# Optimization experiments

Hardware: AMD Instinct MI355X
Metric: run time of the kernel (lower is better)

The kernel has to match this reference:

```python
import jax, jax.numpy as jnp
import numpy as np

EPS = 1e-7  # K.epsilon()

def squash(s):
    # s: [B, J, D]
    sq_norm = jnp.sum(jnp.square(s), axis=-1, keepdims=True)
    scale = sq_norm / (1.0 + sq_norm) / jnp.sqrt(sq_norm + EPS)
    return scale * s

def setup_inputs() -> dict:
    key = jax.random.key(0)
    k1, k2 = jax.random.split(key)
    B, I, Din = 128, 2048, 8
    J, D = 16, 16
    inputs = jax.random.normal(k1, (B, I, Din), dtype=jnp.float32)
    # glorot-uniform-ish scale for W
    limit = np.sqrt(6.0 / (Din + D)).astype(np.float32)
    W = jax.random.uniform(k2, (J, I, D, Din), dtype=jnp.float32, minval=-limit, maxval=limit)
    return {"inputs": inputs, "W": W}

def reference(inputs, W):
    # inputs: [B, I, Din]; W: [J, I, D, Din]
    num_routings = 3
    # inputs_hat[b,j,i,d] = sum_f W[j,i,d,f] * inputs[b,i,f]
    u_hat = jnp.einsum('bif,jidf->bjid', inputs, W)  # [B, J, I, D]
    B, J, I, D = u_hat.shape
    b = jnp.zeros((B, J, I), dtype=u_hat.dtype)
    v = None
    for r in range(num_routings):
        c = jax.nn.softmax(b, axis=1)                 # softmax over output capsules (dim=1)
        s = jnp.einsum('bji,bjid->bjd', c, u_hat)     # weighted sum over input capsules
        v = squash(s)                                 # [B, J, D]
        if r < num_routings - 1:
            b = b + jnp.einsum('bjd,bjid->bji', v, u_hat)  # agreement update
    return v
```

## Files before the change

### kernel.cpp

```cpp
#include <hip/hip_runtime.h>
#include <math.h>

#define B_   128
#define I_   2048
#define F_   8
#define J_   16
#define D_   16
#define JD   256
#define IT   16
#define NIT  (I_/IT)
#define BT   16
#define NBT  (B_/BT)
#define SROW 257

typedef _Float16 f16;
typedef _Float16 f16x8 __attribute__((ext_vector_type(8)));
typedef _Float16 f16x4 __attribute__((ext_vector_type(4)));
typedef float    f32x4 __attribute__((ext_vector_type(4)));

#if defined(__has_builtin)
#  if __has_builtin(__builtin_amdgcn_permlane32_swap)
#    define HAVE_PLS32 1
#  endif
#endif

template <int CTRL>
__device__ __forceinline__ float dpp_add(float v) {
    int t = __builtin_amdgcn_update_dpp(0, __float_as_int(v), CTRL, 0xF, 0xF, true);
    return v + __int_as_float(t);
}
__device__ __forceinline__ float row_sum16(float v) {
    v = dpp_add<0x128>(v);
    v = dpp_add<0x124>(v);
    v = dpp_add<0x122>(v);
    v = dpp_add<0x121>(v);
    return v;
}

__device__ __forceinline__ float fold16(float p) {
    return p + __int_as_float(__builtin_amdgcn_ds_swizzle(__float_as_int(p), 0x401F));
}
__device__ __forceinline__ float fold32(float p) {
#ifdef HAVE_PLS32
    auto r = __builtin_amdgcn_permlane32_swap(__float_as_int(p), __float_as_int(p),
                                              false, false);
    return __int_as_float(r[0]) + __int_as_float(r[1]);
#else
    return p + __shfl_xor(p, 32);
#endif
}

__global__ __launch_bounds__(256) void cvt_f16(const float* __restrict__ W,
                                               const float* __restrict__ x,
                                               f16* __restrict__ Wt,
                                               f16* __restrict__ xt) {
    const size_t NW = (size_t)J_ * I_ * D_ * F_;
    const size_t NX = (size_t)B_ * I_ * F_;
    size_t k = ((size_t)blockIdx.x * 256 + threadIdx.x) * 4;
    if (k < NW) {
        float4 a = *reinterpret_cast<const float4*>(W + k);
        f16x4 h = {(f16)a.x, (f16)a.y, (f16)a.z, (f16)a.w};
        *reinterpret_cast<f16x4*>(Wt + k) = h;
    } else {
        size_t k2 = k - NW;
        if (k2 < NX) {
            float4 a = *reinterpret_cast<const float4*>(x + k2);
            f16x4 h = {(f16)a.x, (f16)a.y, (f16)a.z, (f16)a.w};
            *reinterpret_cast<f16x4*>(xt + k2) = h;
        }
    }
}

template <int PASS>
__global__ __launch_bounds__(256) void caps_pass(
    const f16* __restrict__ Wt,
    const f16* __restrict__ xt,
    const float* __restrict__ vsum,
    f16* __restrict__ sp)
{
    const int it = blockIdx.x, bg = blockIdx.y;
    const int i0 = it * IT, b0 = bg * BT;
    const int t = threadIdx.x;
    const int w = t >> 6, l = t & 63;
    const int lb = l & 15, lq = l >> 4;

    __shared__ f16   xlds[IT][BT][F_];
    __shared__ float cl[PASS ? (J_ * IT * BT) : 1];
    __shared__ float slds[BT * SROW];

    {
        const int b = t >> 4, i = t & 15;
        f16x8 v = *reinterpret_cast<const f16x8*>(
            xt + ((size_t)(b0 + b) * I_ + i0 + i) * F_);
        *reinterpret_cast<f16x8*>(&xlds[i][b][0]) = v;
    }

    const f16* wp[4];
    #pragma unroll
    for (int jj = 0; jj < 4; ++jj)
        wp[jj] = Wt + (((size_t)(w * 4 + jj) * I_ + i0) * D_ + lb) * F_;

    f32x4 zero = {0.f, 0.f, 0.f, 0.f};
    f32x4 sacc[4] = {zero, zero, zero, zero};

    if constexpr (PASS == 1) {
        float4 vr[4];
        #pragma unroll
        for (int jj = 0; jj < 4; ++jj)
            vr[jj] = *reinterpret_cast<const float4*>(
                vsum + (size_t)(b0 + lb) * JD + (w * 4 + jj) * D_ + lq * 4);
        __syncthreads();

        #pragma unroll 4
        for (int il = 0; il < IT; ++il) {
            f16x8 bf = {0, 0, 0, 0, 0, 0, 0, 0};
            if (l < 16) bf = *reinterpret_cast<const f16x8*>(&xlds[il][lb][0]);
            #pragma unroll
            for (int jj = 0; jj < 4; ++jj) {
                f16x8 af = *reinterpret_cast<const f16x8*>(wp[jj] + il * (D_ * F_));
                f32x4 u = __builtin_amdgcn_mfma_f32_16x16x32_f16(af, bf, zero, 0, 0, 0);
                float p = u[0] * vr[jj].x + u[1] * vr[jj].y +
                          u[2] * vr[jj].z + u[3] * vr[jj].w;
                p = fold32(fold16(p));
                if (l < 16) cl[(((w * 4 + jj) * IT) + il) * BT + lb] = p;
            }
        }
        __syncthreads();

        {
            const int i = t >> 4, b = t & 15;
            float e[J_];
            float mx = -1e30f;
            #pragma unroll
            for (int j = 0; j < J_; ++j) {
                e[j] = cl[(j * IT + i) * BT + b];
                mx = fmaxf(mx, e[j]);
            }
            float s = 0.f;
            #pragma unroll
            for (int j = 0; j < J_; ++j) { e[j] = __expf(e[j] - mx); s += e[j]; }
            const float inv = 1.f / s;
            #pragma unroll
            for (int j = 0; j < J_; ++j) cl[(j * IT + i) * BT + b] = e[j] * inv;
        }
        __syncthreads();
    } else {
        __syncthreads();
    }

    #pragma unroll
    for (int m = 0; m < 4; ++m) {
        const int i = m * 4 + lq;
        f16x8 xf = *reinterpret_cast<const f16x8*>(&xlds[i][lb][0]);
        #pragma unroll
        for (int jj = 0; jj < 4; ++jj) {
            f16x8 bf;
            if constexpr (PASS == 1) {
                const float cf = cl[(((w * 4 + jj) * IT) + i) * BT + lb];
                const f16 ch = (f16)cf;
                bf = xf * ch;
            } else {
                bf = xf;
            }
            f16x8 af = *reinterpret_cast<const f16x8*>(wp[jj] + i * (D_ * F_));
            sacc[jj] = __builtin_amdgcn_mfma_f32_16x16x32_f16(af, bf, sacc[jj], 0, 0, 0);
        }
    }

    #pragma unroll
    for (int jj = 0; jj < 4; ++jj) {
        if constexpr (PASS == 0) sacc[jj] *= 0.0625f;
        const int j = w * 4 + jj;
        #pragma unroll
        for (int r = 0; r < 4; ++r)
            slds[lb * SROW + j * D_ + lq * 4 + r] = sacc[jj][r];
    }
    __syncthreads();
    {
        const int b = t >> 4, seg = t & 15;
        float o[16];
        #pragma unroll
        for (int k = 0; k < 16; ++k)
            o[k] = slds[b * SROW + seg * 16 + k];
        f16x8 o0 = {(f16)o[0], (f16)o[1], (f16)o[2],  (f16)o[3],
                    (f16)o[4], (f16)o[5], (f16)o[6],  (f16)o[7]};
        f16x8 o1 = {(f16)o[8], (f16)o[9], (f16)o[10], (f16)o[11],
                    (f16)o[12], (f16)o[13], (f16)o[14], (f16)o[15]};
        f16* dst = sp + ((size_t)it * B_ + b0 + b) * JD + seg * 16;
        *reinterpret_cast<f16x8*>(dst) = o0;
        *reinterpret_cast<f16x8*>(dst + 8) = o1;
    }
}

template <int MODE>
__global__ __launch_bounds__(512) void caps_reduce(
    const f16* __restrict__ sp,
    const float* __restrict__ vA,
    float* __restrict__ vout)
{
    const int b = blockIdx.x;
    const int t = threadIdx.x;
    const int jd = t & 255, h = t >> 8;

    float acc = 0.f;
    const f16* p = sp + ((size_t)(h * 64) * B_ + b) * JD + jd;
    #pragma unroll 16
    for (int i = 0; i < 64; ++i)
        acc += (float)p[(size_t)i * B_ * JD];

    __shared__ float red[256];
    if (h) red[jd] = acc;
    __syncthreads();
    if (!h) {
        acc += red[jd];
        const float sq = row_sum16(acc * acc);
        const float scale = sq / (1.f + sq) * rsqrtf(sq + 1e-7f);
        float v = scale * acc;
        if (MODE == 1) v += vA[(size_t)b * JD + jd];
        vout[(size_t)b * JD + jd] = v;
    }
}

extern "C" void kernel_launch(void* const* d_in, const int* in_sizes, int n_in,
                              void* d_out, int out_size, void* d_ws,
                              size_t ws_size, hipStream_t stream) {
    const float* x = (const float*)d_in[0];
    const float* W = (const float*)d_in[1];
    float* out = (float*)d_out;

    f16* Wt = (f16*)d_ws;
    f16* xt = Wt + (size_t)J_ * I_ * D_ * F_;
    f16* sp = xt + (size_t)B_ * I_ * F_;
    float* vA = (float*)(sp + (size_t)NIT * B_ * JD);
    float* vB = vA + (size_t)B_ * JD;

    const int TOT4 = (int)(((size_t)J_ * I_ * D_ * F_ + (size_t)B_ * I_ * F_) / 4);
    cvt_f16<<<TOT4 / 256, 256, 0, stream>>>(W, x, Wt, xt);

    dim3 grid(NIT, NBT), blk(256);

    caps_pass<0><<<grid, blk, 0, stream>>>(Wt, xt, nullptr, sp);
    caps_reduce<0><<<B_, 512, 0, stream>>>(sp, nullptr, vA);
    caps_pass<1><<<grid, blk, 0, stream>>>(Wt, xt, vA, sp);
    caps_reduce<1><<<B_, 512, 0, stream>>>(sp, vA, vB);
    caps_pass<1><<<grid, blk, 0, stream>>>(Wt, xt, vB, sp);
    caps_reduce<2><<<B_, 512, 0, stream>>>(sp, nullptr, out);
}
```

Measured before the change: 80.28 us.

## Replace partial-sum buffers and reduce kernels with fp32 atomics and fused squash

Each routing pass now accumulates its per-tile s contributions straight into fp32 global buffers with hardware float atomics, instead of writing fp16 partials that a separate reduce kernel then summed. The squash (and the running sum of v across iterations) is recomputed at the start of each pass from the raw s buffers, so only one small final squash kernel remains and a memset clears the accumulators. This cuts two kernel launches and the partial-buffer round trip, but adds atomic contention: 128 tiles add into each element. It also adds redundant squash work in every block and makes the accumulation order nondeterministic.

Result: slower. 214.1 us (+166.8%).

```diff
diff --git a/kernel.cpp b/kernel.cpp
--- a/kernel.cpp
+++ b/kernel.cpp
@@ -11,7 +11,7 @@
 #define NIT  (I_/IT)
 #define BT   16
 #define NBT  (B_/BT)
-#define SROW 257
+#define VROW 260
 
 typedef _Float16 f16;
 typedef _Float16 f16x8 __attribute__((ext_vector_type(8)));
@@ -47,6 +47,14 @@
     return __int_as_float(r[0]) + __int_as_float(r[1]);
 #else
     return p + __shfl_xor(p, 32);
+#endif
+}
+
+__device__ __forceinline__ void atomic_add_f32(float* p, float v) {
+#if defined(__AMDGCN__)
+    asm volatile("global_atomic_add_f32 %0, %1, off" :: "v"(p), "v"(v) : "memory");
+#else
+    atomicAdd(p, v);
 #endif
 }
 
@@ -75,8 +83,9 @@
 __global__ __launch_bounds__(256) void caps_pass(
     const f16* __restrict__ Wt,
     const f16* __restrict__ xt,
-    const float* __restrict__ vsum,
-    f16* __restrict__ sp)
+    const float* __restrict__ vS0,
+    const float* __restrict__ vS1,
+    float* __restrict__ vSo)
 {
     const int it = blockIdx.x, bg = blockIdx.y;
     const int i0 = it * IT, b0 = bg * BT;
@@ -86,7 +95,7 @@
 
     __shared__ f16   xlds[IT][BT][F_];
     __shared__ float cl[PASS ? (J_ * IT * BT) : 1];
-    __shared__ float slds[BT * SROW];
+    __shared__ float vlds[PASS ? (BT * VROW) : 1];
 
     {
         const int b = t >> 4, i = t & 15;
@@ -95,6 +104,45 @@
         *reinterpret_cast<f16x8*>(&xlds[i][b][0]) = v;
     }
 
+    if constexpr (PASS >= 1) {
+        const int b = t >> 4, j = t & 15;
+        const float* p0 = vS0 + (size_t)(b0 + b) * JD + j * D_;
+        float s[16], v[16];
+        #pragma unroll
+        for (int q = 0; q < 4; ++q) {
+            float4 a = *reinterpret_cast<const float4*>(p0 + q * 4);
+            s[q * 4 + 0] = a.x; s[q * 4 + 1] = a.y;
+            s[q * 4 + 2] = a.z; s[q * 4 + 3] = a.w;
+        }
+        float sq = 0.f;
+        #pragma unroll
+        for (int d = 0; d < 16; ++d) sq = fmaf(s[d], s[d], sq);
+        float scale = sq / (1.f + sq) * rsqrtf(sq + 1e-7f);
+        #pragma unroll
+        for (int d = 0; d < 16; ++d) v[d] = scale * s[d];
+        if constexpr (PASS == 2) {
+            const float* p1 = vS1 + (size_t)(b0 + b) * JD + j * D_;
+            #pragma unroll
+            for (int q = 0; q < 4; ++q) {
+                float4 a = *reinterpret_cast<const float4*>(p1 + q * 4);
+                s[q * 4 + 0] = a.x; s[q * 4 + 1] = a.y;
+                s[q * 4 + 2] = a.z; s[q * 4 + 3] = a.w;
+            }
+            sq = 0.f;
+            #pragma unroll
+            for (int d = 0; d < 16; ++d) sq = fmaf(s[d], s[d], sq);
+            scale = sq / (1.f + sq) * rsqrtf(sq + 1e-7f);
+            #pragma unroll
+            for (int d = 0; d < 16; ++d) v[d] += scale * s[d];
+        }
+        #pragma unroll
+        for (int q = 0; q < 4; ++q) {
+            float4 a = {v[q * 4 + 0], v[q * 4 + 1], v[q * 4 + 2], v[q * 4 + 3]};
+            *reinterpret_cast<float4*>(&vlds[b * VROW + j * D_ + q * 4]) = a;
+        }
+    }
+    __syncthreads();
+
     const f16* wp[4];
     #pragma unroll
     for (int jj = 0; jj < 4; ++jj)
@@ -103,13 +151,12 @@
     f32x4 zero = {0.f, 0.f, 0.f, 0.f};
     f32x4 sacc[4] = {zero, zero, zero, zero};
 
-    if constexpr (PASS == 1) {
+    if constexpr (PASS >= 1) {
         float4 vr[4];
         #pragma unroll
         for (int jj = 0; jj < 4; ++jj)
             vr[jj] = *reinterpret_cast<const float4*>(
-                vsum + (size_t)(b0 + lb) * JD + (w * 4 + jj) * D_ + lq * 4);
-        __syncthreads();
+                &vlds[lb * VROW + (w * 4 + jj) * D_ + lq * 4]);
 
         #pragma unroll 4
         for (int il = 0; il < IT; ++il) {
@@ -136,15 +183,13 @@
                 e[j] = cl[(j * IT + i) * BT + b];
                 mx = fmaxf(mx, e[j]);
             }
-            float s = 0.f;
-            #pragma unroll
-            for (int j = 0; j < J_; ++j) { e[j] = __expf(e[j] - mx); s += e[j]; }
-            const float inv = 1.f / s;
+            float ssum = 0.f;
+            #pragma unroll
+            for (int j = 0; j < J_; ++j) { e[j] = __expf(e[j] - mx); ssum += e[j]; }
+            const float inv = 1.f / ssum;
             #pragma unroll
             for (int j = 0; j < J_; ++j) cl[(j * IT + i) * BT + b] = e[j] * inv;
         }
-        __syncthreads();
-    } else {
         __syncthreads();
     }
 
@@ -155,7 +200,7 @@
         #pragma unroll
         for (int jj = 0; jj < 4; ++jj) {
             f16x8 bf;
-            if constexpr (PASS == 1) {
+            if constexpr (PASS >= 1) {
                 const float cf = cl[(((w * 4 + jj) * IT) + i) * BT + lb];
                 const f16 ch = (f16)cf;
                 bf = xf * ch;
@@ -170,55 +215,21 @@
     #pragma unroll
     for (int jj = 0; jj < 4; ++jj) {
         if constexpr (PASS == 0) sacc[jj] *= 0.0625f;
-        const int j = w * 4 + jj;
+        float* base = vSo + (size_t)(b0 + lb) * JD + (w * 4 + jj) * D_ + lq * 4;
         #pragma unroll
         for (int r = 0; r < 4; ++r)
-            slds[lb * SROW + j * D_ + lq * 4 + r] = sacc[jj][r];
-    }
-    __syncthreads();
-    {
-        const int b = t >> 4, seg = t & 15;
-        float o[16];
-        #pragma unroll
-        for (int k = 0; k < 16; ++k)
-            o[k] = slds[b * SROW + seg * 16 + k];
-        f16x8 o0 = {(f16)o[0], (f16)o[1], (f16)o[2],  (f16)o[3],
-                    (f16)o[4], (f16)o[5], (f16)o[6],  (f16)o[7]};
-        f16x8 o1 = {(f16)o[8], (f16)o[9], (f16)o[10], (f16)o[11],
-                    (f16)o[12], (f16)o[13], (f16)o[14], (f16)o[15]};
-        f16* dst = sp + ((size_t)it * B_ + b0 + b) * JD + seg * 16;
-        *reinterpret_cast<f16x8*>(dst) = o0;
-        *reinterpret_cast<f16x8*>(dst + 8) = o1;
-    }
-}
-
-template <int MODE>
-__global__ __launch_bounds__(512) void caps_reduce(
-    const f16* __restrict__ sp,
-    const float* __restrict__ vA,
-    float* __restrict__ vout)
-{
+            atomic_add_f32(base + r, sacc[jj][r]);
+    }
+}
+
+__global__ __launch_bounds__(256) void sq_out(const float* __restrict__ vS2,
+                                              float* __restrict__ out) {
     const int b = blockIdx.x;
     const int t = threadIdx.x;
-    const int jd = t & 255, h = t >> 8;
-
-    float acc = 0.f;
-    const f16* p = sp + ((size_t)(h * 64) * B_ + b) * JD + jd;
-    #pragma unroll 16
-    for (int i = 0; i < 64; ++i)
-        acc += (float)p[(size_t)i * B_ * JD];
-
-    __shared__ float red[256];
-    if (h) red[jd] = acc;
-    __syncthreads();
-    if (!h) {
-        acc += red[jd];
-        const float sq = row_sum16(acc * acc);
-        const float scale = sq / (1.f + sq) * rsqrtf(sq + 1e-7f);
-        float v = scale * acc;
-        if (MODE == 1) v += vA[(size_t)b * JD + jd];
-        vout[(size_t)b * JD + jd] = v;
-    }
+    const float s = vS2[(size_t)b * JD + t];
+    const float sq = row_sum16(s * s);
+    const float scale = sq / (1.f + sq) * rsqrtf(sq + 1e-7f);
+    out[(size_t)b * JD + t] = scale * s;
 }
 
 extern "C" void kernel_launch(void* const* d_in, const int* in_sizes, int n_in,
@@ -230,19 +241,19 @@
 
     f16* Wt = (f16*)d_ws;
     f16* xt = Wt + (size_t)J_ * I_ * D_ * F_;
-    f16* sp = xt + (size_t)B_ * I_ * F_;
-    float* vA = (float*)(sp + (size_t)NIT * B_ * JD);
-    float* vB = vA + (size_t)B_ * JD;
+    float* vS0 = (float*)(xt + (size_t)B_ * I_ * F_);
+    float* vS1 = vS0 + (size_t)B_ * JD;
+    float* vS2 = vS1 + (size_t)B_ * JD;
+
+    hipMemsetAsync(vS0, 0, 3 * (size_t)B_ * JD * sizeof(float), stream);
 
     const int TOT4 = (int)(((size_t)J_ * I_ * D_ * F_ + (size_t)B_ * I_ * F_) / 4);
     cvt_f16<<<TOT4 / 256, 256, 0, stream>>>(W, x, Wt, xt);
 
     dim3 grid(NIT, NBT), blk(256);
 
-    caps_pass<0><<<grid, blk, 0, stream>>>(Wt, xt, nullptr, sp);
-    caps_reduce<0><<<B_, 512, 0, stream>>>(sp, nullptr, vA);
-    caps_pass<1><<<grid, blk, 0, stream>>>(Wt, xt, vA, sp);
-    caps_reduce<1><<<B_, 512, 0, stream>>>(sp, vA, vB);
-    caps_pass<1><<<grid, blk, 0, stream>>>(Wt, xt, vB, sp);
-    caps_reduce<2><<<B_, 512, 0, stream>>>(sp, nullptr, out);
-}
+    caps_pass<0><<<grid, blk, 0, stream>>>(Wt, xt, nullptr, nullptr, vS0);
+    caps_pass<1><<<grid, blk, 0, stream>>>(Wt, xt, vS0, nullptr, vS1);
+    caps_pass<2><<<grid, blk, 0, stream>>>(Wt, xt, vS0, vS1, vS2);
+    sq_out<<<B_, 256, 0, stream>>>(vS2, out);
+}
```

## Halve input-capsule tile, share LDS via union, vectorize split partial reduction

Applied to the files above, without the earlier changes.

The input-capsule tile size becomes a template parameter. When the workspace is large enough, the passes run with 8 capsules per block instead of 16, which doubles the number of blocks. The routing-logit buffer and the output staging buffer now share one LDS union, guarded by an extra barrier, to cut shared-memory use per block. The reduce kernel is split across two blocks per batch row, loads eight f16 values per vector load and reduces 32 groups through LDS. The costs are twice the partial-sum traffic through global memory and a larger workspace requirement; if the workspace is too small, the old 16-capsule tile is used.

Result: no change. 81.59 us (+1.6%).

```diff
diff --git a/kernel.cpp b/kernel.cpp
--- a/kernel.cpp
+++ b/kernel.cpp
@@ -7,8 +7,6 @@
 #define J_   16
 #define D_   16
 #define JD   256
-#define IT   16
-#define NIT  (I_/IT)
 #define BT   16
 #define NBT  (B_/BT)
 #define SROW 257
@@ -71,7 +69,7 @@
     }
 }
 
-template <int PASS>
+template <int IT, int PASS>
 __global__ __launch_bounds__(256) void caps_pass(
     const f16* __restrict__ Wt,
     const f16* __restrict__ xt,
@@ -84,15 +82,24 @@
     const int w = t >> 6, l = t & 63;
     const int lb = l & 15, lq = l >> 4;
 
-    __shared__ f16   xlds[IT][BT][F_];
-    __shared__ float cl[PASS ? (J_ * IT * BT) : 1];
-    __shared__ float slds[BT * SROW];
-
-    {
+    __shared__ f16 xlds[IT][BT][F_];
+    __shared__ union {
+        float cl[J_ * IT * BT];
+        float slds[BT * SROW];
+    } sh;
+
+    if constexpr (IT == 16) {
         const int b = t >> 4, i = t & 15;
         f16x8 v = *reinterpret_cast<const f16x8*>(
             xt + ((size_t)(b0 + b) * I_ + i0 + i) * F_);
         *reinterpret_cast<f16x8*>(&xlds[i][b][0]) = v;
+    } else {
+        if (t < 128) {
+            const int b = t >> 3, i = t & 7;
+            f16x8 v = *reinterpret_cast<const f16x8*>(
+                xt + ((size_t)(b0 + b) * I_ + i0 + i) * F_);
+            *reinterpret_cast<f16x8*>(&xlds[i][b][0]) = v;
+        }
     }
 
     const f16* wp[4];
@@ -122,41 +129,41 @@
                 float p = u[0] * vr[jj].x + u[1] * vr[jj].y +
                           u[2] * vr[jj].z + u[3] * vr[jj].w;
                 p = fold32(fold16(p));
-                if (l < 16) cl[(((w * 4 + jj) * IT) + il) * BT + lb] = p;
+                if (l < 16) sh.cl[(((w * 4 + jj) * IT) + il) * BT + lb] = p;
             }
         }
         __syncthreads();
 
-        {
+        if (t < IT * BT) {
             const int i = t >> 4, b = t & 15;
             float e[J_];
             float mx = -1e30f;
             #pragma unroll
             for (int j = 0; j < J_; ++j) {
-                e[j] = cl[(j * IT + i) * BT + b];
+                e[j] = sh.cl[(j * IT + i) * BT + b];
                 mx = fmaxf(mx, e[j]);
             }
-            float s = 0.f;
-            #pragma unroll
-            for (int j = 0; j < J_; ++j) { e[j] = __expf(e[j] - mx); s += e[j]; }
-            const float inv = 1.f / s;
-            #pragma unroll
-            for (int j = 0; j < J_; ++j) cl[(j * IT + i) * BT + b] = e[j] * inv;
-        }
-        __syncthreads();
-    } else {
-        __syncthreads();
-    }
-
-    #pragma unroll
-    for (int m = 0; m < 4; ++m) {
+            float ssum = 0.f;
+            #pragma unroll
+            for (int j = 0; j < J_; ++j) { e[j] = __expf(e[j] - mx); ssum += e[j]; }
+            const float inv = 1.f / ssum;
+            #pragma unroll
+            for (int j = 0; j < J_; ++j) sh.cl[(j * IT + i) * BT + b] = e[j] * inv;
+        }
+        __syncthreads();
+    } else {
+        __syncthreads();
+    }
+
+    #pragma unroll
+    for (int m = 0; m < IT / 4; ++m) {
         const int i = m * 4 + lq;
         f16x8 xf = *reinterpret_cast<const f16x8*>(&xlds[i][lb][0]);
         #pragma unroll
         for (int jj = 0; jj < 4; ++jj) {
             f16x8 bf;
             if constexpr (PASS == 1) {
-                const float cf = cl[(((w * 4 + jj) * IT) + i) * BT + lb];
+                const float cf = sh.cl[(((w * 4 + jj) * IT) + i) * BT + lb];
                 const f16 ch = (f16)cf;
                 bf = xf * ch;
             } else {
@@ -167,13 +174,15 @@
         }
     }
 
+    __syncthreads();
+
     #pragma unroll
     for (int jj = 0; jj < 4; ++jj) {
         if constexpr (PASS == 0) sacc[jj] *= 0.0625f;
         const int j = w * 4 + jj;
         #pragma unroll
         for (int r = 0; r < 4; ++r)
-            slds[lb * SROW + j * D_ + lq * 4 + r] = sacc[jj][r];
+            sh.slds[lb * SROW + j * D_ + lq * 4 + r] = sacc[jj][r];
     }
     __syncthreads();
     {
@@ -181,7 +190,7 @@
         float o[16];
         #pragma unroll
         for (int k = 0; k < 16; ++k)
-            o[k] = slds[b * SROW + seg * 16 + k];
+            o[k] = sh.slds[b * SROW + seg * 16 + k];
         f16x8 o0 = {(f16)o[0], (f16)o[1], (f16)o[2],  (f16)o[3],
                     (f16)o[4], (f16)o[5], (f16)o[6],  (f16)o[7]};
         f16x8 o1 = {(f16)o[8], (f16)o[9], (f16)o[10], (f16)o[11],
@@ -192,30 +201,39 @@
     }
 }
 
-template <int MODE>
+template <int NITT, int MODE>
 __global__ __launch_bounds__(512) void caps_reduce(
     const f16* __restrict__ sp,
     const float* __restrict__ vA,
     float* __restrict__ vout)
 {
-    const int b = blockIdx.x;
+    const int b = blockIdx.x, jh = blockIdx.y;
     const int t = threadIdx.x;
-    const int jd = t & 255, h = t >> 8;
-
-    float acc = 0.f;
-    const f16* p = sp + ((size_t)(h * 64) * B_ + b) * JD + jd;
-    #pragma unroll 16
-    for (int i = 0; i < 64; ++i)
-        acc += (float)p[(size_t)i * B_ * JD];
-
-    __shared__ float red[256];
-    if (h) red[jd] = acc;
+    const int g = t >> 4, c8 = t & 15;
+    constexpr int ITS = NITT / 32;
+
+    float acc[8] = {0.f, 0.f, 0.f, 0.f, 0.f, 0.f, 0.f, 0.f};
+    const f16* base = sp + ((size_t)(g * ITS) * B_ + b) * JD + jh * 128 + c8 * 8;
+    #pragma unroll
+    for (int k = 0; k < ITS; ++k) {
+        f16x8 v = *reinterpret_cast<const f16x8*>(base + (size_t)k * B_ * JD);
+        #pragma unroll
+        for (int e = 0; e < 8; ++e) acc[e] += (float)v[e];
+    }
+
+    __shared__ float lds[32][128];
+    #pragma unroll
+    for (int e = 0; e < 8; ++e) lds[g][c8 * 8 + e] = acc[e];
     __syncthreads();
-    if (!h) {
-        acc += red[jd];
-        const float sq = row_sum16(acc * acc);
+
+    if (t < 128) {
+        float a = 0.f;
+        #pragma unroll
+        for (int gg = 0; gg < 32; ++gg) a += lds[gg][t];
+        const float sq = row_sum16(a * a);
         const float scale = sq / (1.f + sq) * rsqrtf(sq + 1e-7f);
-        float v = scale * acc;
+        float v = scale * a;
+        const int jd = jh * 128 + t;
         if (MODE == 1) v += vA[(size_t)b * JD + jd];
         vout[(size_t)b * JD + jd] = v;
     }
@@ -228,21 +246,40 @@
     const float* W = (const float*)d_in[1];
     float* out = (float*)d_out;
 
+    const size_t NW = (size_t)J_ * I_ * D_ * F_;
+    const size_t NX = (size_t)B_ * I_ * F_;
+
     f16* Wt = (f16*)d_ws;
-    f16* xt = Wt + (size_t)J_ * I_ * D_ * F_;
-    f16* sp = xt + (size_t)B_ * I_ * F_;
-    float* vA = (float*)(sp + (size_t)NIT * B_ * JD);
-    float* vB = vA + (size_t)B_ * JD;
-
-    const int TOT4 = (int)(((size_t)J_ * I_ * D_ * F_ + (size_t)B_ * I_ * F_) / 4);
-    cvt_f16<<<TOT4 / 256, 256, 0, stream>>>(W, x, Wt, xt);
-
-    dim3 grid(NIT, NBT), blk(256);
-
-    caps_pass<0><<<grid, blk, 0, stream>>>(Wt, xt, nullptr, sp);
-    caps_reduce<0><<<B_, 512, 0, stream>>>(sp, nullptr, vA);
-    caps_pass<1><<<grid, blk, 0, stream>>>(Wt, xt, vA, sp);
-    caps_reduce<1><<<B_, 512, 0, stream>>>(sp, vA, vB);
-    caps_pass<1><<<grid, blk, 0, stream>>>(Wt, xt, vB, sp);
-    caps_reduce<2><<<B_, 512, 0, stream>>>(sp, nullptr, out);
-}
+    f16* xt = Wt + NW;
+    f16* sp = xt + NX;
+
+    const int TOT4 = (int)((NW + NX) / 4);
+
+    const size_t need8 = NW * 2 + NX * 2 +
+                         (size_t)256 * B_ * JD * 2 + 2 * (size_t)B_ * JD * 4;
+    dim3 rgrid(B_, 2), rblk(512);
+
+    if (ws_size >= need8) {
+        float* vA = (float*)(sp + (size_t)256 * B_ * JD);
+        float* vB = vA + (size_t)B_ * JD;
+        dim3 grid(I_ / 8, NBT), blk(256);
+        cvt_f16<<<TOT4 / 256, 256, 0, stream>>>(W, x, Wt, xt);
+        caps_pass<8, 0><<<grid, blk, 0, stream>>>(Wt, xt, nullptr, sp);
+        caps_reduce<256, 0><<<rgrid, rblk, 0, stream>>>(sp, nullptr, vA);
+        caps_pass<8, 1><<<grid, blk, 0, stream>>>(Wt, xt, vA, sp);
+        caps_reduce<256, 1><<<rgrid, rblk, 0, stream>>>(sp, vA, vB);
+        caps_pass<8, 1><<<grid, blk, 0, stream>>>(Wt, xt, vB, sp);
+        caps_reduce<256, 2><<<rgrid, rblk, 0, stream>>>(sp, nullptr, out);
+    } else {
+        float* vA = (float*)(sp + (size_t)128 * B_ * JD);
+        float* vB = vA + (size_t)B_ * JD;
+        dim3 grid(I_ / 16, NBT), blk(256);
+        cvt_f16<<<TOT4 / 256, 256, 0, stream>>>(W, x, Wt, xt);
+        caps_pass<16, 0><<<grid, blk, 0, stream>>>(Wt, xt, nullptr, sp);
+        caps_reduce<128, 0><<<rgrid, rblk, 0, stream>>>(sp, nullptr, vA);
+        caps_pass<16, 1><<<grid, blk, 0, stream>>>(Wt, xt, vA, sp);
+        caps_reduce<128, 1><<<rgrid, rblk, 0, stream>>>(sp, vA, vB);
+        caps_pass<16, 1><<<grid, blk, 0, stream>>>(Wt, xt, vB, sp);
+        caps_reduce<128, 2><<<rgrid, rblk, 0, stream>>>(sp, nullptr, out);
+    }
+}
```
